# Kernel tuning notes

Measured on AMD Instinct MI355X. Metric: run time of the kernel, lower is better.

## Reference

```python
import jax, jax.numpy as jnp
import numpy as np

B, T, D_LAT = 128, 256, 256
N_HIDDEN = 1024
H_SMALL = N_HIDDEN // 2  # 512: lstm1/lstm2 hidden size
H_BIG = N_HIDDEN         # 1024: lstm3 hidden size


def _p(key, shape, scale=0.05):
    return (jax.random.normal(key, shape, dtype=jnp.float32) * scale)


def setup_inputs() -> dict:
    key = jax.random.key(0)
    ks = jax.random.split(key, 16)
    return {
        "X": jax.random.normal(ks[0], (B, T, D_LAT), dtype=jnp.float32),
        # LSTMCell 1: input D_LAT -> hidden H_SMALL (torch layout: [4H, in])
        "W_ih1": _p(ks[1], (4 * H_SMALL, D_LAT)),
        "W_hh1": _p(ks[2], (4 * H_SMALL, H_SMALL)),
        "b_ih1": _p(ks[3], (4 * H_SMALL,)),
        "b_hh1": _p(ks[4], (4 * H_SMALL,)),
        # LSTMCell 2: H_SMALL -> H_SMALL
        "W_ih2": _p(ks[5], (4 * H_SMALL, H_SMALL)),
        "W_hh2": _p(ks[6], (4 * H_SMALL, H_SMALL)),
        "b_ih2": _p(ks[7], (4 * H_SMALL,)),
        "b_hh2": _p(ks[8], (4 * H_SMALL,)),
        # LSTMCell 3: H_SMALL -> H_BIG
        "W_ih3": _p(ks[9], (4 * H_BIG, H_SMALL)),
        "W_hh3": _p(ks[10], (4 * H_BIG, H_BIG)),
        "b_ih3": _p(ks[11], (4 * H_BIG,)),
        "b_hh3": _p(ks[12], (4 * H_BIG,)),
        # Linear: H_BIG -> D_LAT (torch layout: [out, in])
        "W_lin": _p(ks[13], (D_LAT, H_BIG)),
        "b_lin": _p(ks[14], (D_LAT,)),
    }


def _lstm_cell(x, h, c, W_ih, W_hh, b_ih, b_hh):
    # torch.nn.LSTMCell gate order: i, f, g, o
    gates = x @ W_ih.T + b_ih + h @ W_hh.T + b_hh  # [B, 4H]
    i, f, g, o = jnp.split(gates, 4, axis=-1)
    c_new = jax.nn.sigmoid(f) * c + jax.nn.sigmoid(i) * jnp.tanh(g)
    h_new = jax.nn.sigmoid(o) * jnp.tanh(c_new)
    return h_new, c_new


def reference(X, W_ih1, W_hh1, b_ih1, b_hh1,
              W_ih2, W_hh2, b_ih2, b_hh2,
              W_ih3, W_hh3, b_ih3, b_hh3,
              W_lin, b_lin):
    n = X.shape[0]
    z_s = jnp.zeros((n, H_SMALL), dtype=X.dtype)
    z_b = jnp.zeros((n, H_BIG), dtype=X.dtype)
    init = (z_s, z_s, z_s, z_s, z_b, z_b)

    def step(carry, x_t):
        h1, c1, h2, c2, h3, c3 = carry
        h1, c1 = _lstm_cell(x_t, h1, c1, W_ih1, W_hh1, b_ih1, b_hh1)
        h2, c2 = _lstm_cell(h1, h2, c2, W_ih2, W_hh2, b_ih2, b_hh2)
        h3, c3 = _lstm_cell(h2, h3, c3, W_ih3, W_hh3, b_ih3, b_hh3)
        out = h3 @ W_lin.T + b_lin  # [B, D_LAT]
        return (h1, c1, h2, c2, h3, c3), out

    xs = jnp.swapaxes(X, 0, 1)  # [T, B, D_LAT]
    _, outputs = jax.lax.scan(step, init, xs)
    return outputs  # [T, B, D_LAT] == torch.stack(outputs) with future=0
```

## Files before the change

### kernel.cpp

```cpp
#include <hip/hip_runtime.h>
#include <stdint.h>

#define NWG 208

typedef __attribute__((ext_vector_type(8))) short short8;
typedef __attribute__((ext_vector_type(4))) float floatx4;
typedef __attribute__((ext_vector_type(4))) unsigned int uintx4;

static constexpr int Bb = 128, Tt = 256, Dl = 256, Hs = 512, Hb = 1024;
static constexpr int D = 32;
static constexpr int LAG = 4;

static constexpr size_t OFF_FLAGS = 0;
static constexpr size_t OFF_B1  = 1024;
static constexpr size_t OFF_B2  = OFF_B1 + 2048*4;
static constexpr size_t OFF_B3  = OFF_B2 + 2048*4;
static constexpr size_t OFF_BL  = OFF_B3 + 4096*4;
static constexpr size_t OFF_W1  = OFF_BL + 1024;
static constexpr size_t OFF_W2  = OFF_W1 + (size_t)2048*768*2;
static constexpr size_t OFF_W3  = OFF_W2 + (size_t)2048*1024*2;
static constexpr size_t OFF_WL  = OFF_W3 + (size_t)4096*1536*2;
static constexpr size_t FIXED_END = OFF_WL + (size_t)256*1024*2;
static constexpr size_t OFF_H1R  = FIXED_END;
static constexpr size_t OFF_H2R  = OFF_H1R + (size_t)D*Bb*Hs*2;
static constexpr size_t OFF_H3R  = OFF_H2R + (size_t)D*Bb*Hs*2;
static constexpr size_t OFF_XALL = OFF_H3R + (size_t)D*Bb*Hb*2;
static constexpr size_t WS_NEED  = OFF_XALL + (size_t)Tt*Bb*Dl*2;

static constexpr int SMEM_BYTES = 135168;
static constexpr int STG_OFF    = 131072;

__device__ __forceinline__ unsigned short f2bf(float f) {
  unsigned int u = __float_as_uint(f);
  unsigned int r = (u + 0x7fffu + ((u >> 16) & 1u)) >> 16;
  return (unsigned short)r;
}
__device__ __forceinline__ float sigm(float x) { return 1.f/(1.f + __expf(-x)); }
__device__ __forceinline__ float tanh_f(float x) {
  x = fminf(fmaxf(x, -15.f), 15.f);
  float e = __expf(-2.f*x);
  return (1.f - e)/(1.f + e);
}
__device__ __forceinline__ size_t blk_off(int row, int u) {
  return ((size_t)(u >> 5)*8 + (row >> 4))*512 + (size_t)((u & 31) >> 3)*128
       + (size_t)(row & 15)*8 + (u & 7);
}
__device__ __forceinline__ void st_dword_cg(void* p, unsigned int v) {
  asm volatile("global_store_dword %0, %1, off sc0 sc1" :: "v"(p), "v"(v) : "memory");
}
__device__ __forceinline__ void st_b128_cg(void* p, uintx4 v) {
  asm volatile("global_store_dwordx4 %0, %1, off sc0 sc1" :: "v"(p), "v"(v) : "memory");
}
__device__ __forceinline__ void waitcnt_vm0() {
  asm volatile("s_waitcnt vmcnt(0)" ::: "memory");
}

__device__ __forceinline__ void wait_ge(const unsigned int* f, int n, int tgt, int lane) {
  if (tgt <= 0) return;
  const int nl = n >> 2;
  for (;;) {
    int ok = 1;
    if (lane < nl) {
      uintx4 v;
      asm volatile("global_load_dwordx4 %0, %1, off sc0 sc1\n\ts_waitcnt vmcnt(0)"
                   : "=v"(v) : "v"(f + lane*4) : "memory");
      if ((int)v[0] < tgt || (int)v[1] < tgt || (int)v[2] < tgt || (int)v[3] < tgt) ok = 0;
    }
    if (__all(ok)) return;
    __builtin_amdgcn_s_sleep(2);
  }
}

__global__ void lstm_init(
    const float* __restrict__ X,
    const float* __restrict__ Wih1, const float* __restrict__ Whh1,
    const float* __restrict__ bih1, const float* __restrict__ bhh1,
    const float* __restrict__ Wih2, const float* __restrict__ Whh2,
    const float* __restrict__ bih2, const float* __restrict__ bhh2,
    const float* __restrict__ Wih3, const float* __restrict__ Whh3,
    const float* __restrict__ bih3, const float* __restrict__ bhh3,
    const float* __restrict__ Wlin, const float* __restrict__ blin,
    unsigned char* __restrict__ ws)
{
  size_t i0 = (size_t)blockIdx.x*blockDim.x + threadIdx.x;
  size_t np = (size_t)gridDim.x*blockDim.x;

  unsigned int* fl = (unsigned int*)(ws + OFF_FLAGS);
  for (size_t i = i0; i < 256; i += np) fl[i] = 0u;

  float* b1 = (float*)(ws + OFF_B1);
  float* b2 = (float*)(ws + OFF_B2);
  float* b3 = (float*)(ws + OFF_B3);
  float* bl = (float*)(ws + OFF_BL);
  for (size_t i = i0; i < 2048; i += np) b1[i] = bih1[i] + bhh1[i];
  for (size_t i = i0; i < 2048; i += np) b2[i] = bih2[i] + bhh2[i];
  for (size_t i = i0; i < 4096; i += np) b3[i] = bih3[i] + bhh3[i];
  for (size_t i = i0; i < 256;  i += np) bl[i] = blin[i];

  unsigned short* w1 = (unsigned short*)(ws + OFF_W1);
  unsigned short* w2 = (unsigned short*)(ws + OFF_W2);
  unsigned short* w3 = (unsigned short*)(ws + OFF_W3);
  unsigned short* wl = (unsigned short*)(ws + OFF_WL);
  for (size_t i = i0; i < (size_t)2048*768; i += np) {
    size_t r = i/768, k = i - r*768;
    float v = (k < 256) ? Wih1[r*256 + k] : Whh1[r*512 + (k - 256)];
    w1[i] = f2bf(v);
  }
  for (size_t i = i0; i < (size_t)2048*1024; i += np) {
    size_t r = i >> 10, k = i & 1023;
    float v = (k < 512) ? Wih2[r*512 + k] : Whh2[r*512 + (k - 512)];
    w2[i] = f2bf(v);
  }
  for (size_t i = i0; i < (size_t)4096*1536; i += np) {
    size_t r = i/1536, k = i - r*1536;
    float v = (k < 512) ? Wih3[r*512 + k] : Whh3[r*1024 + (k - 512)];
    w3[i] = f2bf(v);
  }
  for (size_t i = i0; i < (size_t)256*1024; i += np) wl[i] = f2bf(Wlin[i]);

  unsigned short* rings = (unsigned short*)(ws + OFF_H1R);
  const size_t nring = (size_t)D*Bb*Hs + (size_t)D*Bb*Hs + (size_t)D*Bb*Hb;
  for (size_t i = i0; i < nring; i += np) rings[i] = 0;

  unsigned short* xall = (unsigned short*)(ws + OFF_XALL);
  for (size_t i = i0; i < (size_t)Tt*Bb*Dl; i += np) {
    size_t t = i >> 15, rem = i & 32767;
    size_t b = rem >> 8, d = rem & 255;
    xall[t*32768 + blk_off((int)b, (int)d)] = f2bf(X[(b*(size_t)Tt + t)*Dl + d]);
  }
}

template<int TYPE>
__device__ __forceinline__ void layer_phase(
    const unsigned short* __restrict__ segA,
    const unsigned short* __restrict__ segB,
    unsigned short* __restrict__ hout,
    unsigned char* __restrict__ smem,
    const float* __restrict__ bias_r,
    float (&creg)[2][2][4],
    int U0, int wv, int lane, int tid)
{
  constexpr int K    = (TYPE==0 ? 768 : TYPE==1 ? 1024 : 1536);
  constexpr int KB1  = (TYPE==0 ? 256 : 512);
  constexpr int MF   = (TYPE==2 ? 1 : 2);
  constexpr int CKS  = (TYPE==2 ? 8 : 4);
  constexpr int NCH  = K/(32*CKS);
  const int l15 = lane & 15;
  const int g   = l15 >> 2;
  const int mbase = (TYPE==2 ? wv*16 : (wv&3)*32);
  const int nfb   = (TYPE==2 ? 0 : (wv>>2)*2);

  const size_t lof = (size_t)(lane >> 4)*128 + (size_t)l15*8;
  const unsigned short* pa[MF];
  const unsigned short* pb[MF];
  #pragma unroll
  for (int mf = 0; mf < MF; ++mf) {
    const size_t rb = (size_t)((mbase >> 4) + mf)*512;
    pa[mf] = segA + rb + lof;
    pb[mf] = segB + rb + lof;
  }
  int rowbyte[2], xr[2];
  #pragma unroll
  for (int nf = 0; nf < 2; ++nf) {
    const int rp = (nfb + nf)*16 + l15;
    rowbyte[nf] = rp*(K*2);
    xr[nf] = (rp & 7) << 4;
  }
  const int klobyte = ((lane >> 4) << 3)*2;

  floatx4 acc[MF][2];
  #pragma unroll
  for (int mf = 0; mf < MF; ++mf)
    #pragma unroll
    for (int nf = 0; nf < 2; ++nf) {
      float bv = bias_r[nf];
      floatx4 b4 = {bv, bv, bv, bv};
      acc[mf][nf] = b4;
    }

  short8 B0[CKS][MF], B1[CKS][MF], B2[CKS][MF];
  auto LOADC = [&](int c, short8 (&A)[CKS][MF]) {
    #pragma unroll
    for (int ks = 0; ks < CKS; ++ks) {
      const int kb = (c*CKS + ks)*32;
      #pragma unroll
      for (int mf = 0; mf < MF; ++mf) {
        const unsigned short* p = (kb < KB1)
            ? pa[mf] + (size_t)(kb >> 5)*4096
            : pb[mf] + (size_t)((kb - KB1) >> 5)*4096;
        A[ks][mf] = *(const short8*)p;
      }
    }
  };
  auto MM = [&](int c, short8 (&A)[CKS][MF]) {
    #pragma unroll
    for (int ks = 0; ks < CKS; ++ks) {
      const int kb = (c*CKS + ks)*32;
      short8 bf[2];
      #pragma unroll
      for (int nf = 0; nf < 2; ++nf)
        bf[nf] = *(const short8*)(smem + rowbyte[nf] + ((kb*2 + klobyte) ^ xr[nf]));
      #pragma unroll
      for (int mf = 0; mf < MF; ++mf)
        #pragma unroll
        for (int nf = 0; nf < 2; ++nf)
          acc[mf][nf] = __builtin_amdgcn_mfma_f32_16x16x32_bf16(A[ks][mf], bf[nf], acc[mf][nf], 0, 0, 0);
    }
  };
  auto LOADB = [&](int c, int b) { if (b == 0) LOADC(c, B0); else if (b == 1) LOADC(c, B1); else LOADC(c, B2); };
  auto MMB   = [&](int c, int b) { if (b == 0) MM(c, B0);    else if (b == 1) MM(c, B1);    else MM(c, B2); };

  LOADB(0, 0); LOADB(1, 1); LOADB(2, 2);
  #pragma unroll
  for (int ch = 0; ch < NCH; ++ch) {
    MMB(ch, ch % 3);
    if (ch + 3 < NCH) LOADB(ch + 3, ch % 3);
  }

  unsigned short* stg = (unsigned short*)(smem + STG_OFF);
  const int a = (U0 & 31) >> 3;
  #pragma unroll
  for (int nf = 0; nf < 2; ++nf) {
    const int u = U0 + (nfb + nf)*4 + (l15 & 3);
    #pragma unroll
    for (int mf = 0; mf < MF; ++mf) {
      float h4[4];
      #pragma unroll
      for (int j = 0; j < 4; ++j) {
        float s0  = acc[mf][nf][j];
        float s4  = __shfl_xor(s0, 4);
        float s8  = __shfl_xor(s0, 8);
        float s12 = __shfl_xor(s0, 12);
        float iv = (g==0)?s0 :(g==1)?s4 :(g==2)?s8 :s12;
        float fv = (g==0)?s4 :(g==1)?s0 :(g==2)?s12:s8;
        float gv = (g==0)?s8 :(g==1)?s12:(g==2)?s0 :s4;
        float ov = (g==0)?s12:(g==1)?s8 :(g==2)?s4 :s0;
        float c  = sigm(fv)*creg[mf][nf][j] + sigm(iv)*tanh_f(gv);
        creg[mf][nf][j] = c;
        h4[j] = sigm(ov)*tanh_f(c);
      }
      float hs = (g==0)?h4[0]:(g==1)?h4[1]:(g==2)?h4[2]:h4[3];
      const int row = mbase + mf*16 + ((lane >> 4) << 2) + g;
      const int c2  = (TYPE==2) ? (row >> 4)
                                : ((row >> 4)*2 + (((u & 31) >> 3) - a));
      stg[c2*128 + (row & 15)*8 + (u & 7)] = f2bf(hs);
    }
  }
  __syncthreads();

  const size_t gbase = (size_t)(U0 >> 5)*4096;
  if (TYPE == 2) {
    if (tid < 128) {
      const int c2 = tid >> 4, w = tid & 15;
      short8 v = *(const short8*)(stg + c2*128 + w*8);
      st_b128_cg(hout + gbase + (size_t)c2*512 + (size_t)a*128 + w*8, *(uintx4*)&v);
    }
  } else {
    if (tid < 256) {
      const int c2 = tid >> 4, w = tid & 15;
      short8 v = *(const short8*)(stg + c2*128 + w*8);
      st_b128_cg(hout + gbase + (size_t)(c2 >> 1)*512 + (size_t)(a + (c2 & 1))*128 + w*8, *(uintx4*)&v);
    }
  }
}

__global__ void __launch_bounds__(512, 2)
lstm_persist(float* __restrict__ out, unsigned char* __restrict__ ws)
{
  extern __shared__ unsigned char smem[];

  __builtin_amdgcn_fence(__ATOMIC_ACQUIRE, "agent");

  const int tid  = threadIdx.x;
  const int lane = tid & 63;
  const int wv   = tid >> 6;
  const int wg   = blockIdx.x;
  const int l15  = lane & 15;

  unsigned int* flags = (unsigned int*)(ws + OFF_FLAGS);
  const float* bias1 = (const float*)(ws + OFF_B1);
  const float* bias2 = (const float*)(ws + OFF_B2);
  const float* bias3 = (const float*)(ws + OFF_B3);
  const float* biasl = (const float*)(ws + OFF_BL);
  const unsigned short* W1 = (const unsigned short*)(ws + OFF_W1);
  const unsigned short* W2 = (const unsigned short*)(ws + OFF_W2);
  const unsigned short* W3 = (const unsigned short*)(ws + OFF_W3);
  const unsigned short* WL = (const unsigned short*)(ws + OFF_WL);
  unsigned short* h1r = (unsigned short*)(ws + OFF_H1R);
  unsigned short* h2r = (unsigned short*)(ws + OFF_H2R);
  unsigned short* h3r = (unsigned short*)(ws + OFF_H3R);
  unsigned short* Xall = (unsigned short*)(ws + OFF_XALL);

  auto slot = [](int t) -> size_t { return (size_t)(t & (D - 1)); };
  const size_t HSs = (size_t)Bb*Hs, HBs = (size_t)Bb*Hb, XBs = (size_t)Bb*Dl;

  int type, U0 = 0, osec = 0, K = 0, WROWS = 0, HGATE = 0;
  const unsigned short* Wg = nullptr; const float* biasp = nullptr;
  if (wg < 32)        { type = 0; U0 = wg*16;        Wg = W1; biasp = bias1; K = 768;  WROWS = 64; HGATE = 512; }
  else if (wg < 64)   { type = 1; U0 = (wg-32)*16;   Wg = W2; biasp = bias2; K = 1024; WROWS = 64; HGATE = 512; }
  else if (wg < 192)  { type = 2; U0 = (wg-64)*8;    Wg = W3; biasp = bias3; K = 1536; WROWS = 32; HGATE = 1024; }
  else                { type = 3; osec = (wg-192)*16; Wg = WL; K = 1024; WROWS = 16; }

  {
    const int rowchunks = K >> 3;
    for (int idx = tid; idx < WROWS*rowchunks; idx += 512) {
      const int rp = idx / rowchunks, kc = idx - rp*rowchunks;
      int R;
      if (type == 3) R = osec + rp;
      else {
        const int c = rp & 15;
        R = (c >> 2)*HGATE + U0 + (rp >> 4)*4 + (c & 3);
      }
      uintx4 v = *(const uintx4*)(Wg + (size_t)R*K + kc*8);
      const int db = rp*(K*2) + ((kc*16) ^ ((rp & 7) << 4));
      *(uintx4*)(smem + db) = v;
    }
  }

  float bias_r[2] = {0.f, 0.f};
  if (type < 3) {
    const int g   = l15 >> 2;
    const int nfb = (type == 2 ? 0 : (wv >> 2)*2);
    #pragma unroll
    for (int nf = 0; nf < 2; ++nf) {
      const int u = U0 + (nfb + nf)*4 + (l15 & 3);
      bias_r[nf] = biasp[g*HGATE + u];
    }
  } else {
    bias_r[0] = biasl[osec + l15];
  }

  float creg[2][2][4];
  #pragma unroll
  for (int a = 0; a < 2; ++a)
    #pragma unroll
    for (int b = 0; b < 2; ++b)
      #pragma unroll
      for (int c = 0; c < 4; ++c) creg[a][b][c] = 0.f;

  __syncthreads();

  for (int t = 0; t < Tt; ++t) {
    if (type == 0) {
      if (wv == 0)      wait_ge(flags + 0, 32, t, lane);
      else if (wv == 1) wait_ge(flags + 32, 32, t - LAG, lane);
    } else if (type == 1) {
      if (wv == 0)      wait_ge(flags + 0, 32, t + 1, lane);
      else if (wv == 1) wait_ge(flags + 32, 32, t, lane);
      else if (wv == 2) wait_ge(flags + 64, 128, t - LAG, lane);
    } else if (type == 2) {
      if (wv == 0)      wait_ge(flags + 32, 32, t + 1, lane);
      else if (wv == 1) wait_ge(flags + 64, 128, t, lane);
      else if (wv == 2) wait_ge(flags + 192, 16, t - LAG, lane);
    } else {
      if (wv == 0)      wait_ge(flags + 64, 128, t + 1, lane);
    }
    __syncthreads();

    if (type == 0) {
      layer_phase<0>(Xall + (size_t)t*XBs,
                     h1r + slot(t-1)*HSs,
                     h1r + slot(t)*HSs,
                     smem, bias_r, creg, U0, wv, lane, tid);
    } else if (type == 1) {
      layer_phase<1>(h1r + slot(t)*HSs,
                     h2r + slot(t-1)*HSs,
                     h2r + slot(t)*HSs,
                     smem, bias_r, creg, U0, wv, lane, tid);
    } else if (type == 2) {
      layer_phase<2>(h2r + slot(t)*HSs,
                     h3r + slot(t-1)*HBs,
                     h3r + slot(t)*HBs,
                     smem, bias_r, creg, U0, wv, lane, tid);
    } else {
      const unsigned short* hA = h3r + slot(t)*HBs;
      const size_t lof = (size_t)(lane >> 4)*128 + (size_t)l15*8;
      const unsigned short* pa0 = hA + (size_t)wv*512 + lof;
      const int rowbyte = l15*2048;
      const int xr = (l15 & 7) << 4;
      const int klobyte = ((lane >> 4) << 3)*2;
      floatx4 oacc;
      { floatx4 b4 = {bias_r[0], bias_r[0], bias_r[0], bias_r[0]}; oacc = b4; }
      short8 A0[4], A1[4];
      auto HLOAD = [&](int c, short8 (&A)[4]) {
        #pragma unroll
        for (int ks = 0; ks < 4; ++ks)
          A[ks] = *(const short8*)(pa0 + (size_t)(c*4 + ks)*4096);
      };
      auto HMM = [&](int c, short8 (&A)[4]) {
        #pragma unroll
        for (int ks = 0; ks < 4; ++ks) {
          const int kb = c*128 + ks*32;
          short8 bw = *(const short8*)(smem + rowbyte + ((kb*2 + klobyte) ^ xr));
          oacc = __builtin_amdgcn_mfma_f32_16x16x32_bf16(A[ks], bw, oacc, 0, 0, 0);
        }
      };
      HLOAD(0, A0);
      #pragma unroll 1
      for (int ch = 0; ch < 8; ch += 2) {
        HLOAD(ch + 1, A1);
        HMM(ch, A0);
        if (ch + 2 < 8) HLOAD(ch + 2, A0);
        HMM(ch + 1, A1);
      }
      const int col = osec + l15;
      const int b0 = wv*16 + ((lane >> 4) << 2);
      #pragma unroll
      for (int j = 0; j < 4; ++j)
        st_dword_cg(out + ((size_t)t*Bb + b0 + j)*Dl + col,
                    __float_as_uint(oacc[j]));
    }

    waitcnt_vm0();
    __syncthreads();
    if (tid == 0) st_dword_cg(flags + wg, (unsigned)(t + 1));
    if ((t & 7) == 7)
      __builtin_amdgcn_fence(__ATOMIC_ACQUIRE, "agent");
  }
}

extern "C" void kernel_launch(void* const* d_in, const int* in_sizes, int n_in,
                              void* d_out, int out_size, void* d_ws, size_t ws_size,
                              hipStream_t stream)
{
  if (ws_size < WS_NEED) return;

  const float* X    = (const float*)d_in[0];
  const float* Wih1 = (const float*)d_in[1];
  const float* Whh1 = (const float*)d_in[2];
  const float* bih1 = (const float*)d_in[3];
  const float* bhh1 = (const float*)d_in[4];
  const float* Wih2 = (const float*)d_in[5];
  const float* Whh2 = (const float*)d_in[6];
  const float* bih2 = (const float*)d_in[7];
  const float* bhh2 = (const float*)d_in[8];
  const float* Wih3 = (const float*)d_in[9];
  const float* Whh3 = (const float*)d_in[10];
  const float* bih3 = (const float*)d_in[11];
  const float* bhh3 = (const float*)d_in[12];
  const float* Wlin = (const float*)d_in[13];
  const float* blin = (const float*)d_in[14];
  unsigned char* ws = (unsigned char*)d_ws;

  lstm_init<<<2048, 256, 0, stream>>>(X, Wih1, Whh1, bih1, bhh1,
                                      Wih2, Whh2, bih2, bhh2,
                                      Wih3, Whh3, bih3, bhh3,
                                      Wlin, blin, ws);
  lstm_persist<<<NWG, 512, SMEM_BYTES, stream>>>((float*)d_out, ws);
}
```

Before: 3.381 ms.

## Split layer-3 K dimension across wave halves with LDS reduction

For the large third LSTM layer, each wave now covers 32 batch rows (two M fragments) over half of K instead of 16 rows over the full K. The two halves reduce partial accumulators through shared memory, and the bias is added only once. This aims to shorten the per-wave serial MFMA chain and improve register reuse of the B fragments on the latency-critical recurrent step. The cost is two extra barriers, LDS traffic for the reduction, and half the waves sitting idle during the gate epilogue.

After: 3.613 ms. +6.9%, slower.

```diff
diff --git a/kernel.cpp b/kernel.cpp
--- a/kernel.cpp
+++ b/kernel.cpp
@@ -28,6 +28,7 @@
 static constexpr size_t WS_NEED  = OFF_XALL + (size_t)Tt*Bb*Dl*2;
 
 static constexpr int SMEM_BYTES = 135168;
+static constexpr int RED_OFF    = 98304;
 static constexpr int STG_OFF    = 131072;
 
 __device__ __forceinline__ unsigned short f2bf(float f) {
@@ -142,13 +143,17 @@
 {
   constexpr int K    = (TYPE==0 ? 768 : TYPE==1 ? 1024 : 1536);
   constexpr int KB1  = (TYPE==0 ? 256 : 512);
-  constexpr int MF   = (TYPE==2 ? 1 : 2);
-  constexpr int CKS  = (TYPE==2 ? 8 : 4);
-  constexpr int NCH  = K/(32*CKS);
+  constexpr int MF   = 2;
+  constexpr int CKS  = 4;
+  constexpr bool KS2 = (TYPE==2);
+  constexpr int KSPAN = KS2 ? (K/2) : K;
+  constexpr int NCH  = KSPAN/(32*CKS);
   const int l15 = lane & 15;
   const int g   = l15 >> 2;
-  const int mbase = (TYPE==2 ? wv*16 : (wv&3)*32);
-  const int nfb   = (TYPE==2 ? 0 : (wv>>2)*2);
+  const int mbase = (wv & 3)*32;
+  const int kq    = KS2 ? (wv >> 2) : 0;
+  const int nfb   = KS2 ? 0 : (wv >> 2)*2;
+  const int k0    = kq * KSPAN;
 
   const size_t lof = (size_t)(lane >> 4)*128 + (size_t)l15*8;
   const unsigned short* pa[MF];
@@ -173,7 +178,7 @@
   for (int mf = 0; mf < MF; ++mf)
     #pragma unroll
     for (int nf = 0; nf < 2; ++nf) {
-      float bv = bias_r[nf];
+      float bv = (KS2 && kq == 1) ? 0.f : bias_r[nf];
       floatx4 b4 = {bv, bv, bv, bv};
       acc[mf][nf] = b4;
     }
@@ -182,7 +187,7 @@
   auto LOADC = [&](int c, short8 (&A)[CKS][MF]) {
     #pragma unroll
     for (int ks = 0; ks < CKS; ++ks) {
-      const int kb = (c*CKS + ks)*32;
+      const int kb = k0 + (c*CKS + ks)*32;
       #pragma unroll
       for (int mf = 0; mf < MF; ++mf) {
         const unsigned short* p = (kb < KB1)
@@ -195,7 +200,7 @@
   auto MM = [&](int c, short8 (&A)[CKS][MF]) {
     #pragma unroll
     for (int ks = 0; ks < CKS; ++ks) {
-      const int kb = (c*CKS + ks)*32;
+      const int kb = k0 + (c*CKS + ks)*32;
       short8 bf[2];
       #pragma unroll
       for (int nf = 0; nf < 2; ++nf)
@@ -217,33 +222,55 @@
     if (ch + 3 < NCH) LOADB(ch + 3, ch % 3);
   }
 
+  if (KS2) {
+    floatx4* red = (floatx4*)(smem + RED_OFF);
+    __syncthreads();
+    if (kq == 1) {
+      #pragma unroll
+      for (int mf = 0; mf < MF; ++mf)
+        #pragma unroll
+        for (int nf = 0; nf < 2; ++nf)
+          red[(((wv & 3)*4 + mf*2 + nf) << 6) + lane] = acc[mf][nf];
+    }
+    __syncthreads();
+    if (kq == 0) {
+      #pragma unroll
+      for (int mf = 0; mf < MF; ++mf)
+        #pragma unroll
+        for (int nf = 0; nf < 2; ++nf)
+          acc[mf][nf] += red[(((wv & 3)*4 + mf*2 + nf) << 6) + lane];
+    }
+  }
+
   unsigned short* stg = (unsigned short*)(smem + STG_OFF);
   const int a = (U0 & 31) >> 3;
-  #pragma unroll
-  for (int nf = 0; nf < 2; ++nf) {
-    const int u = U0 + (nfb + nf)*4 + (l15 & 3);
-    #pragma unroll
-    for (int mf = 0; mf < MF; ++mf) {
-      float h4[4];
-      #pragma unroll
-      for (int j = 0; j < 4; ++j) {
-        float s0  = acc[mf][nf][j];
-        float s4  = __shfl_xor(s0, 4);
-        float s8  = __shfl_xor(s0, 8);
-        float s12 = __shfl_xor(s0, 12);
-        float iv = (g==0)?s0 :(g==1)?s4 :(g==2)?s8 :s12;
-        float fv = (g==0)?s4 :(g==1)?s0 :(g==2)?s12:s8;
-        float gv = (g==0)?s8 :(g==1)?s12:(g==2)?s0 :s4;
-        float ov = (g==0)?s12:(g==1)?s8 :(g==2)?s4 :s0;
-        float c  = sigm(fv)*creg[mf][nf][j] + sigm(iv)*tanh_f(gv);
-        creg[mf][nf][j] = c;
-        h4[j] = sigm(ov)*tanh_f(c);
+  if (!KS2 || kq == 0) {
+    #pragma unroll
+    for (int nf = 0; nf < 2; ++nf) {
+      const int u = U0 + (nfb + nf)*4 + (l15 & 3);
+      #pragma unroll
+      for (int mf = 0; mf < MF; ++mf) {
+        float h4[4];
+        #pragma unroll
+        for (int j = 0; j < 4; ++j) {
+          float s0  = acc[mf][nf][j];
+          float s4  = __shfl_xor(s0, 4);
+          float s8  = __shfl_xor(s0, 8);
+          float s12 = __shfl_xor(s0, 12);
+          float iv = (g==0)?s0 :(g==1)?s4 :(g==2)?s8 :s12;
+          float fv = (g==0)?s4 :(g==1)?s0 :(g==2)?s12:s8;
+          float gv = (g==0)?s8 :(g==1)?s12:(g==2)?s0 :s4;
+          float ov = (g==0)?s12:(g==1)?s8 :(g==2)?s4 :s0;
+          float c  = sigm(fv)*creg[mf][nf][j] + sigm(iv)*tanh_f(gv);
+          creg[mf][nf][j] = c;
+          h4[j] = sigm(ov)*tanh_f(c);
+        }
+        float hs = (g==0)?h4[0]:(g==1)?h4[1]:(g==2)?h4[2]:h4[3];
+        const int row = mbase + mf*16 + ((lane >> 4) << 2) + g;
+        const int c2  = (TYPE==2) ? (row >> 4)
+                                  : ((row >> 4)*2 + (((u & 31) >> 3) - a));
+        stg[c2*128 + (row & 15)*8 + (u & 7)] = f2bf(hs);
       }
-      float hs = (g==0)?h4[0]:(g==1)?h4[1]:(g==2)?h4[2]:h4[3];
-      const int row = mbase + mf*16 + ((lane >> 4) << 2) + g;
-      const int c2  = (TYPE==2) ? (row >> 4)
-                                : ((row >> 4)*2 + (((u & 31) >> 3) - a));
-      stg[c2*128 + (row & 15)*8 + (u & 7)] = f2bf(hs);
     }
   }
   __syncthreads();
```
